# Optimization experiments

Hardware: AMD Instinct MI355X
Metric: run time of the kernel (lower is better)

## Reference

```python
import jax, jax.numpy as jnp
import numpy as np

T, O, K = 256, 64, 16
H, W = 224, 224
D_MODEL, D_OBJ = 768, 2048
GAMMA_INIT = 0.1
OMEGA = 1e-06


def setup_inputs() -> dict:
    key = jax.random.key(0)
    ks = jax.random.split(key, 8)
    obj_feat = jax.random.normal(ks[0], (T, O, D_OBJ), dtype=jnp.float32)
    frame_feat = jax.random.normal(ks[1], (T, D_MODEL), dtype=jnp.float32)
    mark_embeddings = jax.random.normal(ks[2], (K, D_MODEL), dtype=jnp.float32)
    obj_entity = jax.random.randint(ks[3], (T, O), 0, K + 1, dtype=jnp.int32)
    masks = jax.random.randint(ks[4], (T, H, W), 0, K + 1, dtype=jnp.int32)
    # learned params (nn.Linear: y = x @ W.T + b; here stored as [in, out])
    W_obj = jax.random.normal(ks[5], (D_MODEL, D_OBJ), dtype=jnp.float32) / np.sqrt(D_MODEL)
    b_obj = jnp.zeros((D_OBJ,), dtype=jnp.float32)
    W_frame = jax.random.normal(ks[6], (D_MODEL, D_MODEL), dtype=jnp.float32) / np.sqrt(D_MODEL)
    b_frame = jnp.zeros((D_MODEL,), dtype=jnp.float32)
    gamma = jnp.asarray(GAMMA_INIT, dtype=jnp.float32)
    return {
        "obj_feat": obj_feat,
        "frame_feat": frame_feat,
        "mark_embeddings": mark_embeddings,
        "obj_entity": obj_entity,
        "masks": masks,
        "W_obj": W_obj,
        "b_obj": b_obj,
        "W_frame": W_frame,
        "b_frame": b_frame,
        "gamma": gamma,
    }


def reference(obj_feat, frame_feat, mark_embeddings, obj_entity, masks,
              W_obj, b_obj, W_frame, b_frame, gamma):
    # ---- inject_objects: o_hat = o + gamma * P_obj(r_k) (Eq. 4.2) ----
    proj_obj = mark_embeddings @ W_obj + b_obj            # [K, D_OBJ]
    valid = (obj_entity > 0)                              # entity_id == 0 -> no mark
    idx = jnp.clip(obj_entity - 1, 0)                     # [T, O]
    obj_out = obj_feat + gamma * jnp.where(valid[..., None], proj_obj[idx], 0.0)

    # ---- inject_frames: S_t = sum_k (m_k * r_k) / (omega + sum_k m_k) (Eq. 4.3) ----
    Tn, Kn = frame_feat.shape[0], mark_embeddings.shape[0]
    flat = masks.reshape(Tn, -1)                          # [T, H*W]
    seg = (flat + (Kn + 1) * jnp.arange(Tn, dtype=flat.dtype)[:, None]).reshape(-1)
    counts = jax.ops.segment_sum(
        jnp.ones(seg.shape, dtype=jnp.float32), seg, num_segments=Tn * (Kn + 1)
    ).reshape(Tn, Kn + 1)[:, 1:]                          # [T, K] pixel counts per entity
    proj_frame = mark_embeddings @ W_frame + b_frame      # [K, d_model]
    spatial = counts @ proj_frame                         # [T, d_model]
    weight = OMEGA + counts.sum(axis=-1, keepdims=True)   # [T, 1]
    frame_out = frame_feat + gamma * spatial / weight

    return obj_out, frame_out
```

## Files before the change

kernel.cpp:

```cpp
#include <hip/hip_runtime.h>

#define T_N 256
#define O_N 64
#define K_N 16
#define HW_N (224 * 224)
#define DM 768
#define DO 2048
#define OMEGA_F 1e-6f

typedef float f32x4 __attribute__((ext_vector_type(4)));

#define PCOLS 64
#define DSEG 64
#define NSEG (DM / DSEG)
#define NT_O (DO / PCOLS)
#define NT_F (DM / PCOLS)
#define NB_PROJ ((NT_O + NT_F) * NSEG)
#define SUBB 4
#define NB_HIST (T_N * SUBB)
#define NB_OBJ (T_N * O_N / 4)

__global__ __launch_bounds__(256) void proj_kernel(const float* __restrict__ me,
                                                   const float* __restrict__ Wo, const float* __restrict__ bo,
                                                   const float* __restrict__ Wf, const float* __restrict__ bf,
                                                   float* __restrict__ proj_obj, float* __restrict__ proj_frame) {
    __shared__ float partial[4][K_N][PCOLS];
    __shared__ float me_s[K_N * DSEG];
    const int b = blockIdx.x;
    const int tid = threadIdx.x;

    const int tile = b / NSEG, seg = b - tile * NSEG;
    const float* W; const float* bias; float* out; int ld; int j0;
    if (tile < NT_O) { W = Wo; bias = bo; out = proj_obj;   ld = DO; j0 = tile * PCOLS; }
    else             { W = Wf; bias = bf; out = proj_frame; ld = DM; j0 = (tile - NT_O) * PCOLS; }
    const int d0 = seg * DSEG;

    for (int i = tid; i < K_N * DSEG; i += 256) {
        int k = i >> 6, dd = i & 63;
        me_s[i] = me[k * DM + d0 + dd];
    }
    __syncthreads();

    const int jj = tid & (PCOLS - 1);
    const int s  = tid >> 6;
    const int j  = j0 + jj;
    const int db = s * 16;

    float acc[K_N];
    #pragma unroll
    for (int k = 0; k < K_N; ++k) acc[k] = 0.f;

    #pragma unroll
    for (int dd = 0; dd < 16; ++dd) {
        float w = W[(size_t)(d0 + db + dd) * ld + j];
        #pragma unroll
        for (int k = 0; k < K_N; ++k)
            acc[k] += me_s[k * DSEG + db + dd] * w;
    }
    #pragma unroll
    for (int k = 0; k < K_N; ++k) partial[s][k][jj] = acc[k];
    __syncthreads();

    for (int o = tid; o < K_N * PCOLS; o += 256) {
        int k = o >> 6, c = o & 63;
        float v = partial[0][k][c] + partial[1][k][c]
                + partial[2][k][c] + partial[3][k][c];
        if (seg == NSEG - 1) v += bias[j0 + c];
        atomicAdd(&out[k * ld + j0 + c], v);
    }
}

__global__ __launch_bounds__(256) void objhist_kernel(const int* __restrict__ masks,
                                                      float* __restrict__ counts_partial,
                                                      const float* __restrict__ obj_feat,
                                                      const int* __restrict__ obj_entity,
                                                      const float* __restrict__ proj_obj,
                                                      const float* __restrict__ gamma,
                                                      float* __restrict__ obj_out) {
    __shared__ char smem[18496];
    const int b = blockIdx.x;
    const int tid = threadIdx.x;

    if (b < NB_HIST) {
        int* bins = (int*)smem;
        int (*partial2)[17] = (int (*)[17])(smem + 256 * 17 * 4);
        const int t = b >> 2, sub = b & 3;
        int* my = &bins[tid * 17];
        #pragma unroll
        for (int i = 0; i < 17; ++i) my[i] = 0;

        const int4* p = (const int4*)(masks + (size_t)t * HW_N);
        const int n4 = HW_N / 4;
        const int chunk = n4 / SUBB;
        const int end = (sub + 1) * chunk;
        for (int i = sub * chunk + tid; i < end; i += 256) {
            int4 v = p[i];
            my[v.x]++; my[v.y]++; my[v.z]++; my[v.w]++;
        }
        __syncthreads();
        const int bcol = tid & 15, rg = tid >> 4;
        int ssum = 0;
        #pragma unroll
        for (int r = 0; r < 16; ++r) ssum += bins[(rg * 16 + r) * 17 + (bcol + 1)];
        partial2[rg][bcol] = ssum;
        __syncthreads();
        if (tid < 16) {
            int s = 0;
            #pragma unroll
            for (int r = 0; r < 16; ++r) s += partial2[r][tid];
            counts_partial[((size_t)sub * T_N + t) * K_N + tid] = (float)s;
        }
    } else {
        const int wave = tid >> 6;
        const int lane = tid & 63;
        const int row = (b - NB_HIST) * 4 + wave;
        const int e = obj_entity[row];
        const float g = gamma[0];
        const f32x4* __restrict__ src = (const f32x4*)(obj_feat + (size_t)row * DO);
        f32x4* __restrict__ dst = (f32x4*)(obj_out + (size_t)row * DO);
        if (e > 0) {
            const f32x4* __restrict__ pr = (const f32x4*)(proj_obj + (size_t)(e - 1) * DO);
            f32x4 a[8], p[8];
            #pragma unroll
            for (int it = 0; it < 8; ++it) a[it] = src[lane + it * 64];
            #pragma unroll
            for (int it = 0; it < 8; ++it) p[it] = pr[lane + it * 64];
            #pragma unroll
            for (int it = 0; it < 8; ++it) {
                f32x4 r = a[it] + g * p[it];
                __builtin_nontemporal_store(r, &dst[lane + it * 64]);
            }
        } else {
            #pragma unroll
            for (int it = 0; it < 8; ++it) {
                f32x4 a = src[lane + it * 64];
                __builtin_nontemporal_store(a, &dst[lane + it * 64]);
            }
        }
    }
}

__global__ __launch_bounds__(256) void frame_kernel(const float* __restrict__ frame_feat,
                                                    const float* __restrict__ counts_partial,
                                                    const float* __restrict__ proj_frame,
                                                    const float* __restrict__ gamma,
                                                    float* __restrict__ frame_out) {
    __shared__ float c[K_N];
    const int t = blockIdx.x;
    const float g = gamma[0];
    if (threadIdx.x < K_N) {
        float s = 0.f;
        #pragma unroll
        for (int sb = 0; sb < SUBB; ++sb)
            s += counts_partial[((size_t)sb * T_N + t) * K_N + threadIdx.x];
        c[threadIdx.x] = s;
    }
    __syncthreads();
    float tot = 0.f;
    #pragma unroll
    for (int k = 0; k < K_N; ++k) tot += c[k];
    const float inv = g / (OMEGA_F + tot);
    for (int j = threadIdx.x; j < DM; j += 256) {
        float acc = 0.f;
        #pragma unroll
        for (int k = 0; k < K_N; ++k) acc += c[k] * proj_frame[k * DM + j];
        frame_out[t * DM + j] = frame_feat[t * DM + j] + acc * inv;
    }
}

extern "C" void kernel_launch(void* const* d_in, const int* in_sizes, int n_in,
                              void* d_out, int out_size, void* d_ws, size_t ws_size,
                              hipStream_t stream) {
    const float* obj_feat   = (const float*)d_in[0];
    const float* frame_feat = (const float*)d_in[1];
    const float* me         = (const float*)d_in[2];
    const int*   obj_entity = (const int*)d_in[3];
    const int*   masks      = (const int*)d_in[4];
    const float* Wo         = (const float*)d_in[5];
    const float* bo         = (const float*)d_in[6];
    const float* Wf         = (const float*)d_in[7];
    const float* bf         = (const float*)d_in[8];
    const float* gamma      = (const float*)d_in[9];

    float* obj_out   = (float*)d_out;
    float* frame_out = (float*)d_out + (size_t)T_N * O_N * DO;

    float* ws = (float*)d_ws;
    float* proj_obj       = ws;
    float* proj_frame     = ws + 32768;
    float* counts_partial = ws + 32768 + 12288;

    hipMemsetAsync(ws, 0, (size_t)(32768 + 12288) * sizeof(float), stream);

    proj_kernel<<<NB_PROJ, 256, 0, stream>>>(me, Wo, bo, Wf, bf, proj_obj, proj_frame);
    objhist_kernel<<<NB_HIST + NB_OBJ, 256, 0, stream>>>(
        masks, counts_partial, obj_feat, obj_entity, proj_obj, gamma, obj_out);
    frame_kernel<<<T_N, 256, 0, stream>>>(frame_feat, counts_partial, proj_frame, gamma, frame_out);
}
```

Baseline: 67.51 us.

## Replace LDS per-thread histogram with packed register byte counters and wave shuffles

```diff
diff --git a/kernel.cpp b/kernel.cpp
--- a/kernel.cpp
+++ b/kernel.cpp
@@ -77,37 +77,49 @@
                                                       const float* __restrict__ proj_obj,
                                                       const float* __restrict__ gamma,
                                                       float* __restrict__ obj_out) {
-    __shared__ char smem[18496];
+    __shared__ int hist_red[4][16];
     const int b = blockIdx.x;
     const int tid = threadIdx.x;
 
     if (b < NB_HIST) {
-        int* bins = (int*)smem;
-        int (*partial2)[17] = (int (*)[17])(smem + 256 * 17 * 4);
         const int t = b >> 2, sub = b & 3;
-        int* my = &bins[tid * 17];
-        #pragma unroll
-        for (int i = 0; i < 17; ++i) my[i] = 0;
-
+        unsigned c0 = 0, c1 = 0, c2 = 0, c3 = 0;
         const int4* p = (const int4*)(masks + (size_t)t * HW_N);
-        const int n4 = HW_N / 4;
-        const int chunk = n4 / SUBB;
+        const int chunk = HW_N / 4 / SUBB;
         const int end = (sub + 1) * chunk;
         for (int i = sub * chunk + tid; i < end; i += 256) {
             int4 v = p[i];
-            my[v.x]++; my[v.y]++; my[v.z]++; my[v.w]++;
+            #define ACC(val) { int u = (val) - 1; \
+                unsigned inc = ((val) > 0) ? (1u << ((u & 3) << 3)) : 0u; \
+                int q = u >> 2; \
+                c0 += (q == 0) ? inc : 0u; c1 += (q == 1) ? inc : 0u; \
+                c2 += (q == 2) ? inc : 0u; c3 += (q == 3) ? inc : 0u; }
+            ACC(v.x) ACC(v.y) ACC(v.z) ACC(v.w)
+            #undef ACC
+        }
+        unsigned r0 = c0 & 0x00FF00FFu, r1 = (c0 >> 8) & 0x00FF00FFu;
+        unsigned r2 = c1 & 0x00FF00FFu, r3 = (c1 >> 8) & 0x00FF00FFu;
+        unsigned r4 = c2 & 0x00FF00FFu, r5 = (c2 >> 8) & 0x00FF00FFu;
+        unsigned r6 = c3 & 0x00FF00FFu, r7 = (c3 >> 8) & 0x00FF00FFu;
+        #pragma unroll
+        for (int m = 1; m < 64; m <<= 1) {
+            r0 += __shfl_xor(r0, m, 64); r1 += __shfl_xor(r1, m, 64);
+            r2 += __shfl_xor(r2, m, 64); r3 += __shfl_xor(r3, m, 64);
+            r4 += __shfl_xor(r4, m, 64); r5 += __shfl_xor(r5, m, 64);
+            r6 += __shfl_xor(r6, m, 64); r7 += __shfl_xor(r7, m, 64);
+        }
+        const int wave = tid >> 6, lane = tid & 63;
+        if (lane == 0) {
+            int* red = hist_red[wave];
+            red[0]  = r0 & 0xFFFF; red[1]  = r1 & 0xFFFF; red[2]  = r0 >> 16; red[3]  = r1 >> 16;
+            red[4]  = r2 & 0xFFFF; red[5]  = r3 & 0xFFFF; red[6]  = r2 >> 16; red[7]  = r3 >> 16;
+            red[8]  = r4 & 0xFFFF; red[9]  = r5 & 0xFFFF; red[10] = r4 >> 16; red[11] = r5 >> 16;
+            red[12] = r6 & 0xFFFF; red[13] = r7 & 0xFFFF; red[14] = r6 >> 16; red[15] = r7 >> 16;
         }
         __syncthreads();
-        const int bcol = tid & 15, rg = tid >> 4;
-        int ssum = 0;
-        #pragma unroll
-        for (int r = 0; r < 16; ++r) ssum += bins[(rg * 16 + r) * 17 + (bcol + 1)];
-        partial2[rg][bcol] = ssum;
-        __syncthreads();
-        if (tid < 16) {
-            int s = 0;
-            #pragma unroll
-            for (int r = 0; r < 16; ++r) s += partial2[r][tid];
+        if (tid < K_N) {
+            int s = hist_red[0][tid] + hist_red[1][tid]
+                  + hist_red[2][tid] + hist_red[3][tid];
             counts_partial[((size_t)sub * T_N + t) * K_N + tid] = (float)s;
         }
     } else {
```

Measured after the change: 67.82 us. Within noise of the previous version (+0.5%).
